# Kernel tuning notes

Measured on AMD Instinct MI355X. Metric: run time of the kernel, lower is better.

## Reference

```python
import jax, jax.numpy as jnp
import numpy as np

B, S, R, L, E, H, V = 16, 128, 4, 50, 64, 64, 1000
PH1, PH2 = 256, 64


def gru_all(x, Wi, Wh, bi, bh):
    # x: [N, T, D] -> all hidden states [N, T, H]; PyTorch-style GRU cell.
    Hd = Wh.shape[0]
    xw = x @ Wi + bi  # precompute input gates [N, T, 3H]
    def step(h, xt):
        gh = h @ Wh + bh
        xr, xz, xn = jnp.split(xt, 3, axis=-1)
        hr, hz, hn = jnp.split(gh, 3, axis=-1)
        r = jax.nn.sigmoid(xr + hr)
        z = jax.nn.sigmoid(xz + hz)
        n = jnp.tanh(xn + r * hn)
        h = (1.0 - z) * n + z * h
        return h, h
    h0 = jnp.zeros((x.shape[0], Hd), x.dtype)
    _, hs = jax.lax.scan(step, h0, jnp.swapaxes(xw, 0, 1))
    return jnp.swapaxes(hs, 0, 1)


def setup_inputs() -> dict:
    key = jax.random.key(0)
    ks = jax.random.split(key, 24)
    p = lambda k, shp: (jax.random.normal(k, shp, jnp.float32) * 0.05)
    D = E + 1
    return {
        "intra_x": jax.random.randint(ks[0], (B, S), 0, V),
        "inter_his": jax.random.randint(ks[1], (B, S * R, L, 2), 0, 2),
        "inter_r": jax.random.randint(ks[2], (B, S, R, 2), 0, 2),
        "y": jax.random.uniform(ks[3], (B, S), jnp.float32),
        "mask": jnp.ones((B, S), jnp.int32),
        "inter_len": jax.random.randint(ks[4], (B, S, R), 1, L + 1),
        "emb": p(ks[5], (V, E)),
        "Wi_h": p(ks[6], (D, 3 * H)), "Wh_h": p(ks[7], (H, 3 * H)),
        "bi_h": p(ks[8], (3 * H,)), "bh_h": p(ks[9], (3 * H,)),
        "Wi_x": p(ks[10], (D, 3 * H)), "Wh_x": p(ks[11], (H, 3 * H)),
        "bi_x": p(ks[12], (3 * H,)), "bh_x": p(ks[13], (3 * H,)),
        "Wq": p(ks[14], (H, H)),
        "Wo": p(ks[15], (H + H + D, H)), "bo": p(ks[16], (H,)),
        "W1": p(ks[17], (H, PH1)), "b1": p(ks[18], (PH1,)),
        "W2": p(ks[19], (PH1, PH2)), "b2": p(ks[20], (PH2,)),
        "W3": p(ks[21], (PH2, 1)), "b3": p(ks[22], (1,)),
    }


def reference(intra_x, inter_his, inter_r, y, mask, inter_len,
              emb, Wi_h, Wh_h, bi_h, bh_h, Wi_x, Wh_x, bi_x, bh_x,
              Wq, Wo, bo, W1, b1, W2, b2, W3, b3):
    D = E + 1
    # intra-view input: skill embedding + shifted label channel
    x = emb[intra_x]                                    # [B,S,E]
    y_sh = jnp.concatenate([jnp.zeros_like(y[:, :1]), y[:, :-1]], axis=1)[..., None]
    intra = jnp.concatenate([x, y_sh], axis=-1)         # [B,S,E+1]
    # retrieved peer histories / current interactions: embed id + float label
    his = jnp.concatenate([emb[inter_his[..., 0]], inter_his[..., 1:].astype(jnp.float32)], axis=-1)
    his = his.reshape(B, S, R, L, D)
    rcur = jnp.concatenate([emb[inter_r[..., 0]], inter_r[..., 1:].astype(jnp.float32)], axis=-1)  # [B,S,R,E+1]
    # deal_inter: GRU over each peer history, gather state at inter_len-1
    hs = gru_all(his.reshape(B * S * R, L, D), Wi_h, Wh_h, bi_h, bh_h).reshape(B, S, R, L, H)
    idx = (inter_len - 1)[..., None, None]              # [B,S,R,1,1]
    M_rv = jnp.take_along_axis(hs, idx, axis=3).squeeze(3)  # [B,S,R,H]
    M_pv = rcur                                         # [B,S,R,E+1]
    # intra-view GRU over the student's own sequence
    h = gru_all(intra, Wi_x, Wh_x, bi_x, bh_x)          # [B,S,H]
    # inter-view attention over the R retrieved peers
    q = h @ Wq                                          # [B,S,H]
    scores = jnp.einsum('bsh,bsrh->bsr', q, M_rv) / jnp.sqrt(jnp.asarray(H, h.dtype))
    alpha = jax.nn.softmax(scores, axis=-1)             # [B,S,R]
    vals = jnp.concatenate([M_rv, M_pv], axis=-1)       # [B,S,R,H+E+1]
    v = jnp.einsum('bsr,bsrd->bsd', alpha, vals)        # [B,S,H+E+1]
    o = jnp.tanh(jnp.concatenate([h, v], axis=-1) @ Wo + bo)  # [B,S,H]
    # mask is all-ones, so masked_select(o).view(-1, H) == reshape
    o = o.reshape(B * S, H)
    z = jax.nn.relu(o @ W1 + b1)
    z = jax.nn.relu(z @ W2 + b2)
    pred = jax.nn.sigmoid(z @ W3 + b3).squeeze(-1)      # [B*S]
    y_sel = y.reshape(-1)                               # masked_select(y) with ones mask
    return pred, y_sel
```

## Files before the change

kernel.cpp:

```cpp
#include <hip/hip_runtime.h>
#include <hip/hip_bf16.h>
#include <math.h>

#define Bn 16
#define Sn 128
#define Rn 4
#define Ln 50
#define En 64
#define Hn 64
#define Vn 1000
#define G3 192
#define PH1n 256
#define PH2n 64
#define NSEQ (Bn*Sn*Rn)
#define NROW (Bn*Sn)
#define GP 16

typedef short bf16x8 __attribute__((ext_vector_type(8)));
typedef float f32x4  __attribute__((ext_vector_type(4)));

__device__ __forceinline__ unsigned short f2bf(float x) {
    union { float f; unsigned u; } v; v.f = x;
    unsigned r = v.u + 0x7FFF + ((v.u >> 16) & 1);
    return (unsigned short)(r >> 16);
}
__device__ __forceinline__ float bf2f(unsigned short b) {
    union { unsigned u; float f; } v; v.u = ((unsigned)b) << 16; return v.f;
}
__device__ __forceinline__ unsigned cvtpk_bf16(float lo, float hi) {
    unsigned r;
    asm volatile("v_cvt_pk_bf16_f32 %0, %1, %2" : "=v"(r) : "v"(lo), "v"(hi));
    return r;
}
__device__ __forceinline__ float fsig(float x) {
    float e = __builtin_amdgcn_exp2f(-x * 1.442695041f);
    return __builtin_amdgcn_rcpf(1.0f + e);
}
__device__ __forceinline__ float ftanh(float x) {
    float e = __builtin_amdgcn_exp2f(x * 2.885390082f);
    return 1.0f - 2.0f * __builtin_amdgcn_rcpf(e + 1.0f);
}

#define BAR() do { asm volatile("s_waitcnt lgkmcnt(0)" ::: "memory"); \
                   __builtin_amdgcn_s_barrier(); \
                   __builtin_amdgcn_sched_barrier(0); } while (0)

__device__ __forceinline__ void gload3(const float* p, float& a, float& b, float& c) {
    asm volatile("global_load_dword %0, %3, off\n\t"
                 "global_load_dword %1, %3, off offset:256\n\t"
                 "global_load_dword %2, %3, off offset:512"
                 : "=&v"(a), "=&v"(b), "=&v"(c) : "v"(p));
}

#define PK_WQ 0
#define PK_WO 4096
#define PK_W1 18432
#define PK_W2 34816

__global__ __launch_bounds__(192) void precompute_tab(
    const float* __restrict__ emb,
    const float* __restrict__ Wi_h, const float* __restrict__ bi_h,
    const float* __restrict__ bh_h,
    const float* __restrict__ Wi_x, const float* __restrict__ bi_x,
    const float* __restrict__ bh_x,
    const int*   __restrict__ intra_x, const float* __restrict__ y,
    const float* __restrict__ Wq, const float* __restrict__ Wo,
    const float* __restrict__ W1, const float* __restrict__ W2,
    float* __restrict__ pre_h, float* __restrict__ xw,
    unsigned short* __restrict__ packs)
{
    const int bx = blockIdx.x;
    const int j = threadIdx.x;
    __shared__ float e_l[En];
    if (bx < Vn) {
        if (j < En) e_l[j] = emb[bx * En + j];
        __syncthreads();
        float a = bi_h[j] + (j < 128 ? bh_h[j] : 0.0f);
#pragma unroll 8
        for (int k = 0; k < En; ++k) a = fmaf(e_l[k], Wi_h[k * G3 + j], a);
        pre_h[bx * G3 + j] = a;
    } else if (bx < Vn + NROW) {
        const int row = bx - Vn;
        const int id = intra_x[row];
        const float lb = (row & (Sn - 1)) ? y[row - 1] : 0.0f;
        if (j < En) e_l[j] = emb[id * En + j];
        __syncthreads();
        float a = bi_x[j] + (j < 128 ? bh_x[j] : 0.0f);
#pragma unroll 8
        for (int k = 0; k < En; ++k) a = fmaf(e_l[k], Wi_x[k * G3 + j], a);
        a = fmaf(lb, Wi_x[64 * G3 + j], a);
        xw[row * G3 + j] = a;
    } else if (j < 64) {
        const int p = bx - (Vn + NROW);
        const float* W; int KH, N, Kmax, q; unsigned short* dst;
        if (p < 8)       { q = p;      W = Wq; KH = 2; N = 64;  Kmax = 64;  dst = packs + PK_WQ; }
        else if (p < 36) { q = p - 8;  W = Wo; KH = 7; N = 64;  Kmax = 193; dst = packs + PK_WO; }
        else if (p < 68) { q = p - 36; W = W1; KH = 2; N = 256; Kmax = 64;  dst = packs + PK_W1; }
        else             { q = p - 68; W = W2; KH = 8; N = 64;  Kmax = 256; dst = packs + PK_W2; }
        const int nt = q / KH, kh = q - nt * KH;
        const int n  = nt * 16 + (j & 15);
        const int k0 = kh * 32 + (j >> 4) * 8;
#pragma unroll
        for (int i = 0; i < 8; ++i) {
            int k = k0 + i;
            float v = (k < Kmax) ? W[k * N + n] : 0.0f;
            dst[q * 512 + j * 8 + i] = f2bf(v);
        }
    }
}

__global__ __launch_bounds__(256, 2) void gru_fused(
    const float* __restrict__ pre_h, const float* __restrict__ xw,
    const int*   __restrict__ inter_his, const int* __restrict__ inter_len,
    const float* __restrict__ Wh_h, const float* __restrict__ bh_h,
    const float* __restrict__ Wi_h,
    const float* __restrict__ Wh_x, const float* __restrict__ bh_x,
    unsigned short* __restrict__ mrv16, float* __restrict__ h_x)
{
    __shared__ __align__(16) unsigned short h16[2][GP * 64];
    __shared__ int   ids_l[GP][Ln];
    __shared__ float labs_l[GP][Ln];

    const int tid = threadIdx.x;
    const int lane = tid & 63, w = tid >> 6;
    const int n_ = lane & 15, kb = lane >> 4;
    const int jh = w * 16 + n_;
    const int rbase = kb * 4;

    const unsigned arow = (unsigned)(n_ * 128);
    const unsigned ac0  = (unsigned)((kb * 16) ^ ((n_ & 7) << 4));
    const unsigned ac1  = (unsigned)((64 + kb * 16) ^ ((n_ & 7) << 4));
    unsigned woff[4];
#pragma unroll
    for (int q = 0; q < 4; ++q) {
        int r = rbase + q;
        woff[q] = (unsigned)(r * 128 + ((jh * 2) ^ ((r & 7) << 4)));
    }
    for (int i = tid; i < GP * 64; i += 256) h16[0][i] = 0;

    if (blockIdx.x != 0) {
        const int seq0 = ((int)blockIdx.x - 1) * GP;
        for (int i = tid; i < GP * Ln; i += 256) {
            int r = i / Ln, t = i % Ln;
            int base = ((seq0 + r) * Ln + t) * 2;
            ids_l[r][t]  = inter_his[base];
            labs_l[r][t] = (float)inter_his[base + 1];
        }
        bf16x8 bfr[3][2];
#pragma unroll
        for (int g = 0; g < 3; ++g)
#pragma unroll
            for (int kh = 0; kh < 2; ++kh) {
                bf16x8 v;
#pragma unroll
                for (int i = 0; i < 8; ++i)
                    v[i] = (short)f2bf(Wh_h[(kh * 32 + kb * 8 + i) * G3 + g * 64 + jh]);
                bfr[g][kh] = v;
            }
        const float bhn = bh_h[128 + jh];
        const float wlr = Wi_h[64 * G3 + jh];
        const float wlz = Wi_h[64 * G3 + 64 + jh];
        const float wln = Wi_h[64 * G3 + 128 + jh];
        int lenr[4];
#pragma unroll
        for (int q = 0; q < 4; ++q) lenr[q] = inter_len[seq0 + rbase + q];
        float hprev[4] = {0.f, 0.f, 0.f, 0.f};
        float mrvv[4] = {0.f, 0.f, 0.f, 0.f};

        float Ar[4], Az[4], An_[4], Al[4];
        float Br[4], Bz[4], Bn_[4], Bl[4];
#pragma unroll
        for (int q = 0; q < 4; ++q) {
            int id = ids_l[rbase + q][0];
            Al[q] = labs_l[rbase + q][0];
            gload3(pre_h + id * G3 + jh, Ar[q], Az[q], An_[q]);
        }
        __syncthreads();

        auto step = [&](int t, int cur,
                        float (&gr)[4], float (&gz)[4], float (&gn)[4], float (&gl)[4],
                        float (&pr)[4], float (&pz)[4], float (&pn)[4], float (&pl)[4]) {
            const char* rb = (const char*)&h16[cur][0];
            bf16x8 a0 = *(const bf16x8*)(rb + arow + ac0);
            bf16x8 a1 = *(const bf16x8*)(rb + arow + ac1);
            const int tn = (t + 1 < Ln) ? t + 1 : t;
#pragma unroll
            for (int q = 0; q < 4; ++q) {
                int id = ids_l[rbase + q][tn];
                pl[q] = labs_l[rbase + q][tn];
                gload3(pre_h + id * G3 + jh, pr[q], pz[q], pn[q]);
            }
            asm volatile("s_waitcnt vmcnt(12)" ::: "memory");
            __builtin_amdgcn_sched_barrier(0);
            f32x4 c0, c1, c2;
            float xn[4];
#pragma unroll
            for (int q = 0; q < 4; ++q) {
                c0[q] = fmaf(gl[q], wlr, gr[q]);
                c1[q] = fmaf(gl[q], wlz, gz[q]);
                c2[q] = bhn;
                xn[q] = fmaf(gl[q], wln, gn[q]);
            }
            f32x4 acc0 = __builtin_amdgcn_mfma_f32_16x16x32_bf16(a0, bfr[0][0], c0, 0, 0, 0);
            f32x4 acc1 = __builtin_amdgcn_mfma_f32_16x16x32_bf16(a0, bfr[1][0], c1, 0, 0, 0);
            f32x4 acc2 = __builtin_amdgcn_mfma_f32_16x16x32_bf16(a0, bfr[2][0], c2, 0, 0, 0);
            acc0 = __builtin_amdgcn_mfma_f32_16x16x32_bf16(a1, bfr[0][1], acc0, 0, 0, 0);
            acc1 = __builtin_amdgcn_mfma_f32_16x16x32_bf16(a1, bfr[1][1], acc1, 0, 0, 0);
            acc2 = __builtin_amdgcn_mfma_f32_16x16x32_bf16(a1, bfr[2][1], acc2, 0, 0, 0);

            char* wb = (char*)&h16[cur ^ 1][0];
            float hn[4];
#pragma unroll
            for (int q = 0; q < 4; ++q) {
                float rg = fsig(acc0[q]);
                float zg = fsig(acc1[q]);
                float ng = ftanh(fmaf(rg, acc2[q], xn[q]));
                float h  = ng + zg * (hprev[q] - ng);
                hprev[q] = h; hn[q] = h;
                mrvv[q] = (t == lenr[q] - 1) ? h : mrvv[q];
            }
            unsigned u01 = cvtpk_bf16(hn[0], hn[1]);
            unsigned u23 = cvtpk_bf16(hn[2], hn[3]);
            *(unsigned short*)(wb + woff[0]) = (unsigned short)u01;
            *(unsigned short*)(wb + woff[1]) = (unsigned short)(u01 >> 16);
            *(unsigned short*)(wb + woff[2]) = (unsigned short)u23;
            *(unsigned short*)(wb + woff[3]) = (unsigned short)(u23 >> 16);
            BAR();
        };

        for (int t = 0; t < Ln; t += 2) {
            step(t,     0, Ar, Az, An_, Al, Br, Bz, Bn_, Bl);
            step(t + 1, 1, Br, Bz, Bn_, Bl, Ar, Az, An_, Al);
        }
#pragma unroll
        for (int q = 0; q < 4; ++q)
            mrv16[(seq0 + rbase + q) * Hn + jh] = f2bf(mrvv[q]);
    } else {
        bf16x8 bfr[3][2];
#pragma unroll
        for (int g = 0; g < 3; ++g)
#pragma unroll
            for (int kh = 0; kh < 2; ++kh) {
                bf16x8 v;
#pragma unroll
                for (int i = 0; i < 8; ++i)
                    v[i] = (short)f2bf(Wh_x[(kh * 32 + kb * 8 + i) * G3 + g * 64 + jh]);
                bfr[g][kh] = v;
            }
        const float bhn = bh_x[128 + jh];
        float hprev[4] = {0.f, 0.f, 0.f, 0.f};

        const float* q0 = xw + (rbase + 0) * Sn * G3 + jh;
        const float* q1 = xw + (rbase + 1) * Sn * G3 + jh;
        const float* q2 = xw + (rbase + 2) * Sn * G3 + jh;
        const float* q3 = xw + (rbase + 3) * Sn * G3 + jh;
        float* p0 = h_x + (rbase + 0) * Sn * Hn + jh;
        float* p1 = h_x + (rbase + 1) * Sn * Hn + jh;
        float* p2 = h_x + (rbase + 2) * Sn * Hn + jh;
        float* p3 = h_x + (rbase + 3) * Sn * Hn + jh;

        float Ar[4], Az[4], An_[4];
        float Br[4], Bz[4], Bn_[4];
        gload3(q0, Ar[0], Az[0], An_[0]);
        gload3(q1, Ar[1], Az[1], An_[1]);
        gload3(q2, Ar[2], Az[2], An_[2]);
        gload3(q3, Ar[3], Az[3], An_[3]);
        __syncthreads();

        auto istep = [&](int t, int cur,
                         float (&gr)[4], float (&gz)[4], float (&gn)[4],
                         float (&pr)[4], float (&pz)[4], float (&pn)[4]) {
            const char* rb = (const char*)&h16[cur][0];
            bf16x8 a0 = *(const bf16x8*)(rb + arow + ac0);
            bf16x8 a1 = *(const bf16x8*)(rb + arow + ac1);
            if (t + 1 < Sn) { q0 += G3; q1 += G3; q2 += G3; q3 += G3; }
            gload3(q0, pr[0], pz[0], pn[0]);
            gload3(q1, pr[1], pz[1], pn[1]);
            gload3(q2, pr[2], pz[2], pn[2]);
            gload3(q3, pr[3], pz[3], pn[3]);
            asm volatile("s_waitcnt vmcnt(16)" ::: "memory");
            __builtin_amdgcn_sched_barrier(0);
            f32x4 c0 = {gr[0], gr[1], gr[2], gr[3]};
            f32x4 c1 = {gz[0], gz[1], gz[2], gz[3]};
            f32x4 c2 = {bhn, bhn, bhn, bhn};
            f32x4 acc0 = __builtin_amdgcn_mfma_f32_16x16x32_bf16(a0, bfr[0][0], c0, 0, 0, 0);
            f32x4 acc1 = __builtin_amdgcn_mfma_f32_16x16x32_bf16(a0, bfr[1][0], c1, 0, 0, 0);
            f32x4 acc2 = __builtin_amdgcn_mfma_f32_16x16x32_bf16(a0, bfr[2][0], c2, 0, 0, 0);
            acc0 = __builtin_amdgcn_mfma_f32_16x16x32_bf16(a1, bfr[0][1], acc0, 0, 0, 0);
            acc1 = __builtin_amdgcn_mfma_f32_16x16x32_bf16(a1, bfr[1][1], acc1, 0, 0, 0);
            acc2 = __builtin_amdgcn_mfma_f32_16x16x32_bf16(a1, bfr[2][1], acc2, 0, 0, 0);

            char* wb = (char*)&h16[cur ^ 1][0];
            float hn[4];
#pragma unroll
            for (int q = 0; q < 4; ++q) {
                float rg = fsig(acc0[q]);
                float zg = fsig(acc1[q]);
                float ng = ftanh(fmaf(rg, acc2[q], gn[q]));
                float h  = ng + zg * (hprev[q] - ng);
                hprev[q] = h; hn[q] = h;
            }
            unsigned u01 = cvtpk_bf16(hn[0], hn[1]);
            unsigned u23 = cvtpk_bf16(hn[2], hn[3]);
            *(unsigned short*)(wb + woff[0]) = (unsigned short)u01;
            *(unsigned short*)(wb + woff[1]) = (unsigned short)(u01 >> 16);
            *(unsigned short*)(wb + woff[2]) = (unsigned short)u23;
            *(unsigned short*)(wb + woff[3]) = (unsigned short)(u23 >> 16);
            *p0 = hn[0]; p0 += Hn;
            *p1 = hn[1]; p1 += Hn;
            *p2 = hn[2]; p2 += Hn;
            *p3 = hn[3]; p3 += Hn;
            BAR();
        };

        for (int t = 0; t < Sn; t += 2) {
            istep(t,     0, Ar, Az, An_, Br, Bz, Bn_);
            istep(t + 1, 1, Br, Bz, Bn_, Ar, Az, An_);
        }
    }
}

__global__ __launch_bounds__(256) void attn_mlp(
    const float* __restrict__ h_x, const unsigned short* __restrict__ mrv16,
    const float* __restrict__ emb, const int* __restrict__ inter_r,
    const float* __restrict__ y,
    const unsigned short* __restrict__ packs,
    const float* __restrict__ bo, const float* __restrict__ b1,
    const float* __restrict__ b2,
    const float* __restrict__ W3, const float* __restrict__ b3,
    float* __restrict__ out)
{
    const int r0 = blockIdx.x * 16;
    const int tid = threadIdx.x;
    const int lane = tid & 63, w = tid >> 6;
    const int n_ = lane & 15, kb = lane >> 4;
    const unsigned sw = (unsigned)((n_ & 7) << 4);

    __shared__ __align__(16) char aauxB[16 * 512];
    __shared__ __align__(16) char olB[16 * 128];
    __shared__ __align__(16) char z1B[16 * 512];
    __shared__ float Mlf[16][4][65];
    __shared__ float qs[16][68];
    __shared__ float z2f[16][68];
    __shared__ float scl[16][4], al[16][4], rlab[16][4];
    __shared__ int   rid[16][4];

    const unsigned short* pWq = packs + PK_WQ;
    const unsigned short* pWo = packs + PK_WO;
    const unsigned short* pW1 = packs + PK_W1;
    const unsigned short* pW2 = packs + PK_W2;

    for (int i = tid; i < 16 * 96; i += 256) {
        int rr = i / 96, d = 32 + (i % 96);
        ((unsigned*)aauxB)[rr * 128 + d] = 0;
    }
    {
        int rr = tid >> 4, c4 = (tid & 15) * 4;
        float4 hv = *(const float4*)(h_x + (r0 + rr) * Hn + c4);
        unsigned lo = cvtpk_bf16(hv.x, hv.y), hi = cvtpk_bf16(hv.z, hv.w);
        unsigned off = (unsigned)(rr * 512) + (((unsigned)(2 * c4)) ^ ((rr & 7) << 4));
        *(unsigned*)(aauxB + off) = lo;
        *(unsigned*)(aauxB + off + 4) = hi;
    }
    for (int i = tid; i < 4096; i += 256) {
        int rr = i >> 8, rem = i & 255, r = rem >> 6, k = rem & 63;
        Mlf[rr][r][k] = bf2f(mrv16[((r0 + rr) * Rn + r) * Hn + k]);
    }
    if (tid < 64) {
        int rr = tid >> 2, r = tid & 3;
        rid[rr][r]  = inter_r[((r0 + rr) * Rn + r) * 2];
        rlab[rr][r] = (float)inter_r[((r0 + rr) * Rn + r) * 2 + 1];
    }
    __syncthreads();

    {
        bf16x8 a0 = *(const bf16x8*)(aauxB + n_ * 512 + ((0 * 64 + kb * 16) ^ sw));
        bf16x8 a1 = *(const bf16x8*)(aauxB + n_ * 512 + ((1 * 64 + kb * 16) ^ sw));
        bf16x8 b0 = *(const bf16x8*)(pWq + (w * 2 + 0) * 512 + lane * 8);
        bf16x8 b1v = *(const bf16x8*)(pWq + (w * 2 + 1) * 512 + lane * 8);
        f32x4 z4 = {0.f, 0.f, 0.f, 0.f};
        f32x4 qa = __builtin_amdgcn_mfma_f32_16x16x32_bf16(a0, b0, z4, 0, 0, 0);
        qa = __builtin_amdgcn_mfma_f32_16x16x32_bf16(a1, b1v, qa, 0, 0, 0);
#pragma unroll
        for (int q = 0; q < 4; ++q) qs[kb * 4 + q][w * 16 + n_] = qa[q];
    }
    __syncthreads();

    if (tid < 64) {
        int rr = tid >> 2, r = tid & 3;
        float a = 0.f;
#pragma unroll 8
        for (int k = 0; k < 64; ++k) a = fmaf(qs[rr][k], Mlf[rr][r][k], a);
        scl[rr][r] = a * 0.125f;
    }
    __syncthreads();
    if (tid < 16) {
        float m = fmaxf(fmaxf(scl[tid][0], scl[tid][1]), fmaxf(scl[tid][2], scl[tid][3]));
        float s = 0.f, e[4];
#pragma unroll
        for (int r = 0; r < 4; ++r) {
            e[r] = __builtin_amdgcn_exp2f((scl[tid][r] - m) * 1.442695041f); s += e[r];
        }
        float inv = __builtin_amdgcn_rcpf(s);
#pragma unroll
        for (int r = 0; r < 4; ++r) al[tid][r] = e[r] * inv;
    }
    __syncthreads();

    if (tid < 129) {
#pragma unroll 4
        for (int rr = 0; rr < 16; ++rr) {
            float a = 0.f;
#pragma unroll
            for (int r = 0; r < 4; ++r) {
                float val;
                if (tid < 64)       val = Mlf[rr][r][tid];
                else if (tid < 128) val = emb[rid[rr][r] * En + (tid - 64)];
                else                val = rlab[rr][r];
                a = fmaf(al[rr][r], val, a);
            }
            unsigned off = (unsigned)(rr * 512) + (((unsigned)(2 * (64 + tid))) ^ ((rr & 7) << 4));
            *(unsigned short*)(aauxB + off) = f2bf(a);
        }
    }
    __syncthreads();

    {
        f32x4 acc = {0.f, 0.f, 0.f, 0.f};
#pragma unroll
        for (int kh = 0; kh < 7; ++kh) {
            bf16x8 a = *(const bf16x8*)(aauxB + n_ * 512 + ((kh * 64 + kb * 16) ^ sw));
            bf16x8 b = *(const bf16x8*)(pWo + (w * 7 + kh) * 512 + lane * 8);
            acc = __builtin_amdgcn_mfma_f32_16x16x32_bf16(a, b, acc, 0, 0, 0);
        }
        float bov = bo[w * 16 + n_];
#pragma unroll
        for (int q = 0; q < 4; ++q) {
            int row = kb * 4 + q;
            float o = ftanh(acc[q] + bov);
            unsigned off = (unsigned)(row * 128) + (((unsigned)(2 * (w * 16 + n_))) ^ ((row & 7) << 4));
            *(unsigned short*)(olB + off) = f2bf(o);
        }
    }
    __syncthreads();

    {
        bf16x8 a0 = *(const bf16x8*)(olB + n_ * 128 + ((0 * 64 + kb * 16) ^ sw));
        bf16x8 a1 = *(const bf16x8*)(olB + n_ * 128 + ((1 * 64 + kb * 16) ^ sw));
#pragma unroll
        for (int jj = 0; jj < 4; ++jj) {
            bf16x8 bb0 = *(const bf16x8*)(pW1 + ((w * 4 + jj) * 2 + 0) * 512 + lane * 8);
            bf16x8 bb1 = *(const bf16x8*)(pW1 + ((w * 4 + jj) * 2 + 1) * 512 + lane * 8);
            f32x4 z4 = {0.f, 0.f, 0.f, 0.f};
            f32x4 acc = __builtin_amdgcn_mfma_f32_16x16x32_bf16(a0, bb0, z4, 0, 0, 0);
            acc = __builtin_amdgcn_mfma_f32_16x16x32_bf16(a1, bb1, acc, 0, 0, 0);
            float b1v = b1[w * 64 + jj * 16 + n_];
#pragma unroll
            for (int q = 0; q < 4; ++q) {
                int row = kb * 4 + q;
                float z = fmaxf(acc[q] + b1v, 0.0f);
                unsigned off = (unsigned)(row * 512) +
                               (((unsigned)(2 * (w * 64 + jj * 16 + n_))) ^ ((row & 7) << 4));
                *(unsigned short*)(z1B + off) = f2bf(z);
            }
        }
    }
    __syncthreads();

    {
        f32x4 acc = {0.f, 0.f, 0.f, 0.f};
#pragma unroll
        for (int kh = 0; kh < 8; ++kh) {
            bf16x8 a = *(const bf16x8*)(z1B + n_ * 512 + ((kh * 64 + kb * 16) ^ sw));
            bf16x8 b = *(const bf16x8*)(pW2 + (w * 8 + kh) * 512 + lane * 8);
            acc = __builtin_amdgcn_mfma_f32_16x16x32_bf16(a, b, acc, 0, 0, 0);
        }
        float b2v = b2[w * 16 + n_];
#pragma unroll
        for (int q = 0; q < 4; ++q)
            z2f[kb * 4 + q][w * 16 + n_] = fmaxf(acc[q] + b2v, 0.0f);
    }
    __syncthreads();

    if (tid < 16) {
        float a = b3[0];
#pragma unroll 8
        for (int k = 0; k < 64; ++k) a = fmaf(z2f[tid][k], W3[k], a);
        out[r0 + tid] = fsig(a);
        out[NROW + r0 + tid] = y[r0 + tid];
    }
}

extern "C" void kernel_launch(void* const* d_in, const int* in_sizes, int n_in,
                              void* d_out, int out_size, void* d_ws, size_t ws_size,
                              hipStream_t stream) {
    const int*   intra_x   = (const int*)d_in[0];
    const int*   inter_his = (const int*)d_in[1];
    const int*   inter_r   = (const int*)d_in[2];
    const float* y         = (const float*)d_in[3];
    const int*   inter_len = (const int*)d_in[5];
    const float* emb  = (const float*)d_in[6];
    const float* Wi_h = (const float*)d_in[7];
    const float* Wh_h = (const float*)d_in[8];
    const float* bi_h = (const float*)d_in[9];
    const float* bh_h = (const float*)d_in[10];
    const float* Wi_x = (const float*)d_in[11];
    const float* Wh_x = (const float*)d_in[12];
    const float* bi_x = (const float*)d_in[13];
    const float* bh_x = (const float*)d_in[14];
    const float* Wq = (const float*)d_in[15];
    const float* Wo = (const float*)d_in[16];
    const float* bo = (const float*)d_in[17];
    const float* W1 = (const float*)d_in[18];
    const float* b1 = (const float*)d_in[19];
    const float* W2 = (const float*)d_in[20];
    const float* b2 = (const float*)d_in[21];
    const float* W3 = (const float*)d_in[22];
    const float* b3 = (const float*)d_in[23];

    float* out = (float*)d_out;
    float* ws  = (float*)d_ws;
    float*          pre_h = ws;
    float*          xw    = ws + 192000;
    unsigned short* mrv16 = (unsigned short*)(ws + 585216);
    float*          h_x   = ws + 847360;
    unsigned short* packs = (unsigned short*)(ws + 978432);

    precompute_tab<<<Vn + NROW + 100, 192, 0, stream>>>(
        emb, Wi_h, bi_h, bh_h, Wi_x, bi_x, bh_x, intra_x, y,
        Wq, Wo, W1, W2, pre_h, xw, packs);
    gru_fused<<<1 + NSEQ / GP, 256, 0, stream>>>(pre_h, xw, inter_his, inter_len,
                                                 Wh_h, bh_h, Wi_h,
                                                 Wh_x, bh_x,
                                                 mrv16, h_x);
    attn_mlp<<<NROW / 16, 256, 0, stream>>>(h_x, mrv16, emb, inter_r, y,
                                            packs, bo, b1, b2, W3, b3, out);
}
```

Measured before the change: 82.72 us.

## Pack two 16-sequence GRU groups per 512-thread block and split intra GRU

The GRU kernel now runs 512-thread blocks, each holding two independent 16-sequence wave groups with their own double-buffered LDS hidden state, which halves the inter-view block count. The intra-view block is split across the two groups, each handling 8 of the 16 student sequences, with half of the rows masked out of the stores. This is meant to shorten the serial critical path of the long 128-step intra GRU and improve occupancy and scheduling. The cost is that the block-wide barriers now couple both groups, and the wider block may constrain register allocation.

```diff
diff --git a/kernel.cpp b/kernel.cpp
--- a/kernel.cpp
+++ b/kernel.cpp
@@ -14,7 +14,6 @@
 #define PH2n 64
 #define NSEQ (Bn*Sn*Rn)
 #define NROW (Bn*Sn)
-#define GP 16
 
 typedef short bf16x8 __attribute__((ext_vector_type(8)));
 typedef float f32x4  __attribute__((ext_vector_type(4)));
@@ -109,7 +108,7 @@
     }
 }
 
-__global__ __launch_bounds__(256, 2) void gru_fused(
+__global__ __launch_bounds__(512, 2) void gru_fused(
     const float* __restrict__ pre_h, const float* __restrict__ xw,
     const int*   __restrict__ inter_his, const int* __restrict__ inter_len,
     const float* __restrict__ Wh_h, const float* __restrict__ bh_h,
@@ -117,14 +116,15 @@
     const float* __restrict__ Wh_x, const float* __restrict__ bh_x,
     unsigned short* __restrict__ mrv16, float* __restrict__ h_x)
 {
-    __shared__ __align__(16) unsigned short h16[2][GP * 64];
-    __shared__ int   ids_l[GP][Ln];
-    __shared__ float labs_l[GP][Ln];
+    __shared__ __align__(16) unsigned short h16[2][2][1024];
+    __shared__ int   ids_l[32][Ln];
+    __shared__ float labs_l[32][Ln];
 
     const int tid = threadIdx.x;
     const int lane = tid & 63, w = tid >> 6;
+    const int wg = w >> 2, wl = w & 3;
     const int n_ = lane & 15, kb = lane >> 4;
-    const int jh = w * 16 + n_;
+    const int jh = wl * 16 + n_;
     const int rbase = kb * 4;
 
     const unsigned arow = (unsigned)(n_ * 128);
@@ -136,13 +136,14 @@
         int r = rbase + q;
         woff[q] = (unsigned)(r * 128 + ((jh * 2) ^ ((r & 7) << 4)));
     }
-    for (int i = tid; i < GP * 64; i += 256) h16[0][i] = 0;
+    for (int i = tid; i < 4096; i += 512) (&h16[0][0][0])[i] = 0;
 
     if (blockIdx.x != 0) {
-        const int seq0 = ((int)blockIdx.x - 1) * GP;
-        for (int i = tid; i < GP * Ln; i += 256) {
+        const int blk0 = ((int)blockIdx.x - 1) * 32;
+        const int seq0 = blk0 + wg * 16;
+        for (int i = tid; i < 32 * Ln; i += 512) {
             int r = i / Ln, t = i % Ln;
-            int base = ((seq0 + r) * Ln + t) * 2;
+            int base = ((blk0 + r) * Ln + t) * 2;
             ids_l[r][t]  = inter_his[base];
             labs_l[r][t] = (float)inter_his[base + 1];
         }
@@ -161,6 +162,7 @@
         const float wlr = Wi_h[64 * G3 + jh];
         const float wlz = Wi_h[64 * G3 + 64 + jh];
         const float wln = Wi_h[64 * G3 + 128 + jh];
+        const int ridx = wg * 16 + rbase;
         int lenr[4];
 #pragma unroll
         for (int q = 0; q < 4; ++q) lenr[q] = inter_len[seq0 + rbase + q];
@@ -169,25 +171,26 @@
 
         float Ar[4], Az[4], An_[4], Al[4];
         float Br[4], Bz[4], Bn_[4], Bl[4];
+        __syncthreads();
 #pragma unroll
         for (int q = 0; q < 4; ++q) {
-            int id = ids_l[rbase + q][0];
-            Al[q] = labs_l[rbase + q][0];
+            int id = ids_l[ridx + q][0];
+            Al[q] = labs_l[ridx + q][0];
             gload3(pre_h + id * G3 + jh, Ar[q], Az[q], An_[q]);
         }
-        __syncthreads();
+        asm volatile("s_waitcnt vmcnt(0)" ::: "memory");
 
         auto step = [&](int t, int cur,
                         float (&gr)[4], float (&gz)[4], float (&gn)[4], float (&gl)[4],
                         float (&pr)[4], float (&pz)[4], float (&pn)[4], float (&pl)[4]) {
-            const char* rb = (const char*)&h16[cur][0];
+            const char* rb = (const char*)&h16[wg][cur][0];
             bf16x8 a0 = *(const bf16x8*)(rb + arow + ac0);
             bf16x8 a1 = *(const bf16x8*)(rb + arow + ac1);
             const int tn = (t + 1 < Ln) ? t + 1 : t;
 #pragma unroll
             for (int q = 0; q < 4; ++q) {
-                int id = ids_l[rbase + q][tn];
-                pl[q] = labs_l[rbase + q][tn];
+                int id = ids_l[ridx + q][tn];
+                pl[q] = labs_l[ridx + q][tn];
                 gload3(pre_h + id * G3 + jh, pr[q], pz[q], pn[q]);
             }
             asm volatile("s_waitcnt vmcnt(12)" ::: "memory");
@@ -208,7 +211,7 @@
             acc1 = __builtin_amdgcn_mfma_f32_16x16x32_bf16(a1, bfr[1][1], acc1, 0, 0, 0);
             acc2 = __builtin_amdgcn_mfma_f32_16x16x32_bf16(a1, bfr[2][1], acc2, 0, 0, 0);
 
-            char* wb = (char*)&h16[cur ^ 1][0];
+            char* wb = (char*)&h16[wg][cur ^ 1][0];
             float hn[4];
 #pragma unroll
             for (int q = 0; q < 4; ++q) {
@@ -248,16 +251,22 @@
                 bfr[g][kh] = v;
             }
         const float bhn = bh_x[128 + jh];
+        const bool act = (kb < 2);
         float hprev[4] = {0.f, 0.f, 0.f, 0.f};
-
-        const float* q0 = xw + (rbase + 0) * Sn * G3 + jh;
-        const float* q1 = xw + (rbase + 1) * Sn * G3 + jh;
-        const float* q2 = xw + (rbase + 2) * Sn * G3 + jh;
-        const float* q3 = xw + (rbase + 3) * Sn * G3 + jh;
-        float* p0 = h_x + (rbase + 0) * Sn * Hn + jh;
-        float* p1 = h_x + (rbase + 1) * Sn * Hn + jh;
-        float* p2 = h_x + (rbase + 2) * Sn * Hn + jh;
-        float* p3 = h_x + (rbase + 3) * Sn * Hn + jh;
+        int sc[4];
+#pragma unroll
+        for (int q = 0; q < 4; ++q) {
+            int s = wg * 8 + rbase + q;
+            sc[q] = (s < 16) ? s : 15;
+        }
+        const float* q0 = xw + sc[0] * Sn * G3 + jh;
+        const float* q1 = xw + sc[1] * Sn * G3 + jh;
+        const float* q2 = xw + sc[2] * Sn * G3 + jh;
+        const float* q3 = xw + sc[3] * Sn * G3 + jh;
+        float* p0 = h_x + sc[0] * Sn * Hn + jh;
+        float* p1 = h_x + sc[1] * Sn * Hn + jh;
+        float* p2 = h_x + sc[2] * Sn * Hn + jh;
+        float* p3 = h_x + sc[3] * Sn * Hn + jh;
 
         float Ar[4], Az[4], An_[4];
         float Br[4], Bz[4], Bn_[4];
@@ -270,7 +279,7 @@
         auto istep = [&](int t, int cur,
                          float (&gr)[4], float (&gz)[4], float (&gn)[4],
                          float (&pr)[4], float (&pz)[4], float (&pn)[4]) {
-            const char* rb = (const char*)&h16[cur][0];
+            const char* rb = (const char*)&h16[wg][cur][0];
             bf16x8 a0 = *(const bf16x8*)(rb + arow + ac0);
             bf16x8 a1 = *(const bf16x8*)(rb + arow + ac1);
             if (t + 1 < Sn) { q0 += G3; q1 += G3; q2 += G3; q3 += G3; }
@@ -290,7 +299,7 @@
             acc1 = __builtin_amdgcn_mfma_f32_16x16x32_bf16(a1, bfr[1][1], acc1, 0, 0, 0);
             acc2 = __builtin_amdgcn_mfma_f32_16x16x32_bf16(a1, bfr[2][1], acc2, 0, 0, 0);
 
-            char* wb = (char*)&h16[cur ^ 1][0];
+            char* wb = (char*)&h16[wg][cur ^ 1][0];
             float hn[4];
 #pragma unroll
             for (int q = 0; q < 4; ++q) {
@@ -306,10 +315,13 @@
             *(unsigned short*)(wb + woff[1]) = (unsigned short)(u01 >> 16);
             *(unsigned short*)(wb + woff[2]) = (unsigned short)u23;
             *(unsigned short*)(wb + woff[3]) = (unsigned short)(u23 >> 16);
-            *p0 = hn[0]; p0 += Hn;
-            *p1 = hn[1]; p1 += Hn;
-            *p2 = hn[2]; p2 += Hn;
-            *p3 = hn[3]; p3 += Hn;
+            if (act) {
+                *p0 = hn[0];
+                *p1 = hn[1];
+                *p2 = hn[2];
+                *p3 = hn[3];
+            }
+            p0 += Hn; p1 += Hn; p2 += Hn; p3 += Hn;
             BAR();
         };
 
@@ -529,7 +541,7 @@
     precompute_tab<<<Vn + NROW + 100, 192, 0, stream>>>(
         emb, Wi_h, bi_h, bh_h, Wi_x, bi_x, bh_x, intra_x, y,
         Wq, Wo, W1, W2, pre_h, xw, packs);
-    gru_fused<<<1 + NSEQ / GP, 256, 0, stream>>>(pre_h, xw, inter_his, inter_len,
+    gru_fused<<<1 + NSEQ / 32, 512, 0, stream>>>(pre_h, xw, inter_his, inter_len,
                                                  Wh_h, bh_h, Wi_h,
                                                  Wh_x, bh_x,
                                                  mrv16, h_x);
```

Measured after the change: 104.5 us. 26.3% more time.
